# Kernel tuning notes

Hardware: AMD Instinct MI355X
Metric: run time of the kernel (lower is better)

Reference implementation:

```python
import jax, jax.numpy as jnp
import numpy as np

BS, L, D, N, K = 2048, 100, 256, 16, 32
M_CONST = 2
NEG = -1e9


def setup_inputs() -> dict:
    key = jax.random.key(0)
    ks = jax.random.split(key, 6)
    hist = jax.random.normal(ks[0], (BS, L, D), dtype=jnp.float32)
    hist_mask = jnp.ones((BS, L), dtype=jnp.float32)  # passed but unused by PolyAttention (faithful)
    cand = jax.random.normal(ks[1], (BS, N, D), dtype=jnp.float32)
    num_interests = jax.random.randint(ks[2], (BS,), 1, K + 1, dtype=jnp.int32)
    cat_counts = jax.random.randint(ks[3], (BS,), 1, 21, dtype=jnp.int32)
    W_poly = jax.random.normal(ks[4], (D, D), dtype=jnp.float32) * (1.0 / np.sqrt(D))
    context_codes = jax.random.normal(ks[5], (K, D), dtype=jnp.float32) * (1.0 / np.sqrt(D))
    return {
        "history_news_representations": hist,
        "history_mask": hist_mask,
        "candidate_news_representations": cand,
        "num_extracted_interests": num_interests,
        "unique_category_counts": cat_counts,
        "W_poly": W_poly,
        "context_codes": context_codes,
    }


def _forward(hist, hist_mask, cand, num_interests, cat_counts, W_poly, context_codes):
    # --- PolyAttention ---
    proj = jnp.tanh(jnp.einsum("bld,ed->ble", hist, W_poly))        # [bs, L, ccd]
    weights = jnp.einsum("ble,ke->bkl", proj, context_codes)         # [bs, K, L]
    cc_mask = jnp.arange(K)[None, :] < num_interests[:, None]        # [bs, K]
    weights = jnp.where(cc_mask[:, :, None], weights, NEG)
    weights = jax.nn.softmax(weights, axis=2)
    weights = jnp.nan_to_num(weights, nan=0.0, posinf=0.0, neginf=0.0)
    interests = jnp.einsum("bkl,bld->bkd", weights, hist)            # [bs, K, d]

    # --- InterestCandidateAttention over all N candidates at once ---
    aw = jnp.einsum("bkd,bnd->bnk", interests, cand)                 # [bs, N, K]
    dyn_K = jnp.ceil(jnp.log2(M_CONST * cat_counts.astype(jnp.float32))).astype(jnp.int32)
    dyn_K = jnp.clip(dyn_K, 1, K)                                    # [bs]
    # rank of each entry in descending order along K
    order = jnp.argsort(-aw, axis=-1)
    rank = jnp.argsort(order, axis=-1)                               # [bs, N, K]
    topk_mask = (rank < dyn_K[:, None, None]).astype(aw.dtype)
    masked = aw * topk_mask
    user = jnp.einsum("bnk,bkd->bnd", masked, interests)             # [bs, N, d]
    return user


def reference(history_news_representations, history_mask, candidate_news_representations,
              num_extracted_interests, unique_category_counts, W_poly, context_codes):
    return _forward(history_news_representations, history_mask, candidate_news_representations,
                    num_extracted_interests, unique_category_counts, W_poly, context_codes)
```

## Files before the change

### kernel.cpp

```cpp
#include <hip/hip_runtime.h>
#include <math.h>

#define NEGV (-1e9f)

typedef _Float16 half8 __attribute__((ext_vector_type(8)));
typedef float f32x4 __attribute__((ext_vector_type(4)));


__device__ inline float tanh_fast(float x) {
    float t = __expf(2.0f * x);
    float r = __builtin_amdgcn_rcpf(t + 1.0f);
    return fmaf(-2.0f, r, 1.0f);
}

__device__ inline void split8(const float4 a, const float4 b, half8& h, half8& m) {
    const float* pa = (const float*)&a;
    const float* pb = (const float*)&b;
    #pragma unroll
    for (int q = 0; q < 4; ++q) {
        float x = pa[q];
        _Float16 hi = (_Float16)x;
        h[q] = hi; m[q] = (_Float16)(x - (float)hi);
    }
    #pragma unroll
    for (int q = 0; q < 4; ++q) {
        float x = pb[q];
        _Float16 hi = (_Float16)x;
        h[4+q] = hi; m[4+q] = (_Float16)(x - (float)hi);
    }
}

__global__ __launch_bounds__(256)
void k_prep(const float* __restrict__ W, const float* __restrict__ cc,
            half8* __restrict__ Wf, half8* __restrict__ Cf)
{
    int slot = blockIdx.x * 256 + threadIdx.x;
    if (slot < 8192) {
        int kt = slot >> 10;
        int ct = (slot >> 6) & 15;
        int lane = slot & 63;
        int e = ct * 16 + (lane & 15);
        int g = lane >> 4;
        const float* src = &W[(size_t)e * 256 + kt * 32 + g * 8];
        float4 a = *(const float4*)src;
        float4 b = *(const float4*)(src + 4);
        half8 h, m;
        split8(a, b, h, m);
        Wf[((kt * 2 + 0) * 16 + ct) * 64 + lane] = h;
        Wf[((kt * 2 + 1) * 16 + ct) * 64 + lane] = m;
    } else if (slot < 9216) {
        int s = slot - 8192;
        int lane = s & 63;
        int ct = (s >> 6) & 1;
        int et = s >> 7;
        int k2 = ct * 16 + (lane & 15);
        int g = lane >> 4;
        const float* src = &cc[(size_t)k2 * 256 + et * 32 + g * 8];
        float4 a = *(const float4*)src;
        float4 b = *(const float4*)(src + 4);
        half8 h, m;
        split8(a, b, h, m);
        Cf[((et * 2 + 0) * 2 + ct) * 64 + lane] = h;
        Cf[((et * 2 + 1) * 2 + ct) * 64 + lane] = m;
    }
}

__global__ __launch_bounds__(256, 2)
void k_proj_logits(const float* __restrict__ hist, const half8* __restrict__ Wf,
                   const half8* __restrict__ Cf, float* __restrict__ logits)
{
    __shared__ float Pj[128][68];

    const int tid  = threadIdx.x;
    const int lane = tid & 63;
    const int w    = tid >> 6;
    const int wr   = w >> 1, wc = w & 1;
    const int g    = lane >> 4;
    const int r    = lane & 15;
    const size_t rowBase = (size_t)blockIdx.x * 128;

    f32x4 acc[4][8];
    #pragma unroll
    for (int i = 0; i < 4; ++i)
        #pragma unroll
        for (int j = 0; j < 8; ++j) acc[i][j] = (f32x4)(0.0f);

    const float* aPtr = &hist[(rowBase + (size_t)wr * 64 + r) * 256 + g * 8];

    float4 a0[4], a1[4];
    #pragma unroll
    for (int rt = 0; rt < 4; ++rt) {
        const float* s = aPtr + rt * (16 * 256);
        a0[rt] = *(const float4*)s;
        a1[rt] = *(const float4*)(s + 4);
    }

    #pragma unroll
    for (int kt = 0; kt < 8; ++kt) {
        half8 Ah[4], Am[4];
        #pragma unroll
        for (int rt = 0; rt < 4; ++rt)
            split8(a0[rt], a1[rt], Ah[rt], Am[rt]);
        if (kt < 7) {
            #pragma unroll
            for (int rt = 0; rt < 4; ++rt) {
                const float* s = aPtr + rt * (16 * 256) + (kt + 1) * 32;
                a0[rt] = *(const float4*)s;
                a1[rt] = *(const float4*)(s + 4);
            }
        }
        #pragma unroll
        for (int ct = 0; ct < 8; ++ct) {
            int ctg = wc * 8 + ct;
            half8 Bh = Wf[(size_t)((kt * 2 + 0) * 16 + ctg) * 64 + lane];
            half8 Bm = Wf[(size_t)((kt * 2 + 1) * 16 + ctg) * 64 + lane];
            #pragma unroll
            for (int rt = 0; rt < 4; ++rt) {
                acc[rt][ct] = __builtin_amdgcn_mfma_f32_16x16x32_f16(Ah[rt], Bh, acc[rt][ct], 0, 0, 0);
                acc[rt][ct] = __builtin_amdgcn_mfma_f32_16x16x32_f16(Ah[rt], Bm, acc[rt][ct], 0, 0, 0);
                acc[rt][ct] = __builtin_amdgcn_mfma_f32_16x16x32_f16(Am[rt], Bh, acc[rt][ct], 0, 0, 0);
            }
        }
    }

    f32x4 acc2[2][2];
    #pragma unroll
    for (int i = 0; i < 2; ++i)
        #pragma unroll
        for (int j = 0; j < 2; ++j) acc2[i][j] = (f32x4)(0.0f);

    #pragma unroll
    for (int ec = 0; ec < 4; ++ec) {
        __syncthreads();
        if (wc == (ec >> 1)) {
            #pragma unroll
            for (int rt = 0; rt < 4; ++rt) {
                #pragma unroll
                for (int c4i = 0; c4i < 4; ++c4i) {
                    int ctm = (ec & 1) * 4 + c4i;
                    f32x4 t = acc[rt][ctm];
                    int el = c4i * 16 + r;
                    int rb = 64 * wr + rt * 16 + g * 4;
                    #pragma unroll
                    for (int i = 0; i < 4; ++i)
                        Pj[rb + i][el] = tanh_fast(t[i]);
                }
            }
        }
        __syncthreads();
        #pragma unroll
        for (int ks = 0; ks < 2; ++ks) {
            half8 Ah2[2], Am2[2];
            #pragma unroll
            for (int rt2 = 0; rt2 < 2; ++rt2) {
                const float* src = &Pj[32 * w + rt2 * 16 + r][ks * 32 + g * 8];
                float4 p0 = *(const float4*)src;
                float4 p1 = *(const float4*)(src + 4);
                split8(p0, p1, Ah2[rt2], Am2[rt2]);
            }
            int et = ec * 2 + ks;
            #pragma unroll
            for (int ct = 0; ct < 2; ++ct) {
                half8 Bh = Cf[((et * 2 + 0) * 2 + ct) * 64 + lane];
                half8 Bm = Cf[((et * 2 + 1) * 2 + ct) * 64 + lane];
                #pragma unroll
                for (int rt2 = 0; rt2 < 2; ++rt2) {
                    acc2[rt2][ct] = __builtin_amdgcn_mfma_f32_16x16x32_f16(Ah2[rt2], Bh, acc2[rt2][ct], 0, 0, 0);
                    acc2[rt2][ct] = __builtin_amdgcn_mfma_f32_16x16x32_f16(Ah2[rt2], Bm, acc2[rt2][ct], 0, 0, 0);
                    acc2[rt2][ct] = __builtin_amdgcn_mfma_f32_16x16x32_f16(Am2[rt2], Bh, acc2[rt2][ct], 0, 0, 0);
                }
            }
        }
    }
    #pragma unroll
    for (int rt2 = 0; rt2 < 2; ++rt2)
        #pragma unroll
        for (int ct = 0; ct < 2; ++ct)
            #pragma unroll
            for (int i = 0; i < 4; ++i) {
                size_t grow = rowBase + 32 * w + rt2 * 16 + g * 4 + i;
                logits[grow * 32 + ct * 16 + r] = acc2[rt2][ct][i];
            }
}

__global__ __launch_bounds__(256, 3)
void k_attn(const float* __restrict__ hist, const float* __restrict__ cand,
            const int* __restrict__ numi, const int* __restrict__ catc,
            const float* __restrict__ logits, float* __restrict__ out)
{
    __shared__ float wT[100][36];
    __shared__ float ints[32][260];
    __shared__ float aws[16][36];
    __shared__ float maw[16][36];

    const int tid = threadIdx.x;
    const int b = blockIdx.x;
    const int num = numi[b];

    for (int idx = tid; idx < 3200; idx += 256) {
        int l = idx >> 5;
        int k = idx & 31;
        wT[l][k] = logits[(size_t)b * 3200 + idx];
    }
    __syncthreads();

    {
        const int k = tid >> 3;
        const int lg = tid & 7;
        const bool valid = k < num;
        float vals[13];
        float m = -INFINITY;
        #pragma unroll
        for (int i = 0; i < 13; ++i) {
            int l = lg + 8 * i;
            if (l < 100) {
                float v = valid ? wT[l][k] : NEGV;
                vals[i] = v;
                m = fmaxf(m, v);
            }
        }
        #pragma unroll
        for (int off = 1; off < 8; off <<= 1)
            m = fmaxf(m, __shfl_xor(m, off, 8));
        float s = 0.0f;
        #pragma unroll
        for (int i = 0; i < 13; ++i) {
            int l = lg + 8 * i;
            if (l < 100) {
                float e = expf(vals[i] - m);
                s += e;
                wT[l][k] = e;
            }
        }
        #pragma unroll
        for (int off = 1; off < 8; off <<= 1)
            s += __shfl_xor(s, off, 8);
        float inv = 1.0f / s;
        #pragma unroll
        for (int i = 0; i < 13; ++i) {
            int l = lg + 8 * i;
            if (l < 100) wT[l][k] *= inv;
        }
    }
    __syncthreads();

    {
        const int dq = tid & 63;
        const int kh = tid >> 6;
        float4 a4[8];
        #pragma unroll
        for (int kk = 0; kk < 8; ++kk) { a4[kk].x = a4[kk].y = a4[kk].z = a4[kk].w = 0.0f; }
        const float4* hrow = (const float4*)&hist[(size_t)b * 25600] + dq;
        #pragma unroll 4
        for (int l = 0; l < 100; ++l) {
            float4 hv = hrow[(size_t)l * 64];
            float4 w0 = *(const float4*)&wT[l][8 * kh];
            float4 w1 = *(const float4*)&wT[l][8 * kh + 4];
            float wv[8] = {w0.x, w0.y, w0.z, w0.w, w1.x, w1.y, w1.z, w1.w};
            #pragma unroll
            for (int kk = 0; kk < 8; ++kk) {
                a4[kk].x = fmaf(wv[kk], hv.x, a4[kk].x);
                a4[kk].y = fmaf(wv[kk], hv.y, a4[kk].y);
                a4[kk].z = fmaf(wv[kk], hv.z, a4[kk].z);
                a4[kk].w = fmaf(wv[kk], hv.w, a4[kk].w);
            }
        }
        #pragma unroll
        for (int kk = 0; kk < 8; ++kk)
            *(float4*)&ints[8 * kh + kk][4 * dq] = a4[kk];
    }
    __syncthreads();

    {
        const int n = tid & 15;
        const int kq = tid >> 4;
        const float4* cg = (const float4*)&cand[((size_t)b * 16 + n) * 256];
        const float4* i0 = (const float4*)&ints[kq][0];
        const float4* i1 = (const float4*)&ints[kq + 16][0];
        float s0 = 0.0f, s1 = 0.0f;
        for (int q = 0; q < 64; ++q) {
            float4 cv = cg[q];
            float4 v0 = i0[q];
            float4 v1 = i1[q];
            s0 += v0.x * cv.x + v0.y * cv.y + v0.z * cv.z + v0.w * cv.w;
            s1 += v1.x * cv.x + v1.y * cv.y + v1.z * cv.z + v1.w * cv.w;
        }
        aws[n][kq] = s0;
        aws[n][kq + 16] = s1;
    }
    __syncthreads();

    {
        int c = catc[b];
        int dynK = 32 - __clz(2 * c - 1);
        const int k = tid & 31;
        const int n1 = tid >> 5;
        #pragma unroll
        for (int h = 0; h < 2; ++h) {
            int n = n1 + 8 * h;
            float a = aws[n][k];
            int cnt = 0;
            #pragma unroll
            for (int j = 0; j < 32; ++j) {
                float aj = aws[n][j];
                cnt += (aj > a) || (aj == a && j < k);
            }
            maw[n][k] = (cnt < dynK) ? a : 0.0f;
        }
    }
    __syncthreads();

    {
        const int dd = tid & 63;
        const int ng = tid >> 6;
        float4 acc4[4];
        #pragma unroll
        for (int nn = 0; nn < 4; ++nn) { acc4[nn].x = acc4[nn].y = acc4[nn].z = acc4[nn].w = 0.0f; }
        for (int k = 0; k < 32; ++k) {
            float4 iv = *(const float4*)&ints[k][4 * dd];
            #pragma unroll
            for (int nn = 0; nn < 4; ++nn) {
                float m = maw[4 * ng + nn][k];
                acc4[nn].x = fmaf(m, iv.x, acc4[nn].x);
                acc4[nn].y = fmaf(m, iv.y, acc4[nn].y);
                acc4[nn].z = fmaf(m, iv.z, acc4[nn].z);
                acc4[nn].w = fmaf(m, iv.w, acc4[nn].w);
            }
        }
        #pragma unroll
        for (int nn = 0; nn < 4; ++nn) {
            *(float4*)&out[((size_t)b * 16 + 4 * ng + nn) * 256 + 4 * dd] = acc4[nn];
        }
    }
}

extern "C" void kernel_launch(void* const* d_in, const int* in_sizes, int n_in,
                              void* d_out, int out_size, void* d_ws, size_t ws_size,
                              hipStream_t stream) {
    const float* hist = (const float*)d_in[0];
    const float* cand = (const float*)d_in[2];
    const int*   numi = (const int*)d_in[3];
    const int*   catc = (const int*)d_in[4];
    const float* W    = (const float*)d_in[5];
    const float* cc   = (const float*)d_in[6];
    float* out = (float*)d_out;
    float* logits = (float*)d_ws;
    const size_t LOG_BYTES = 26214400;
    const size_t WF_BYTES = 262144;
    const size_t CF_BYTES = 32768;
    char* fragBase = (ws_size >= LOG_BYTES + WF_BYTES + CF_BYTES)
                     ? ((char*)d_ws + LOG_BYTES)
                     : (char*)d_out;
    half8* Wf = (half8*)fragBase;
    half8* Cf = (half8*)(fragBase + WF_BYTES);

    k_prep<<<36, 256, 0, stream>>>(W, cc, Wf, Cf);
    k_proj_logits<<<1600, 256, 0, stream>>>(hist, Wf, Cf, logits);
    k_attn<<<2048, 256, 0, stream>>>(hist, cand, numi, catc, logits, out);
}
```

Before: 265.7 us.

## Double-buffer W tiles in LDS via async global_load_lds in projection GEMM

The projection kernel now streams the pre-split fp16 W_poly tiles into a 64KB double-buffered LDS region with direct global-to-LDS loads, prefetching the next k-tile while MFMAs consume the current one. Previously each wave read the B fragments straight from global memory. The A-operand register prefetch is also double-buffered through a macro-expanded loop with explicit waitcnt and barriers. The enlarged shared buffer may reduce occupancy. Separately, the interest-aggregation loop unroll goes from 4 to 10.

Measured after the change: 243.3 us. -8.4%, faster.

```diff
diff --git a/kernel.cpp b/kernel.cpp
--- a/kernel.cpp
+++ b/kernel.cpp
@@ -28,6 +28,12 @@
         _Float16 hi = (_Float16)x;
         h[4+q] = hi; m[4+q] = (_Float16)(x - (float)hi);
     }
+}
+
+__device__ inline void gload_lds16(const void* g, void* lds) {
+    __builtin_amdgcn_global_load_lds(
+        (const __attribute__((address_space(1))) unsigned int*)g,
+        (__attribute__((address_space(3))) unsigned int*)lds, 16, 0, 0);
 }
 
 __global__ __launch_bounds__(256)
@@ -65,11 +71,53 @@
     }
 }
 
+#define K1_BODY(KT, CURBUF, RS0, RS1, RD0, RD1, LAST)                              \
+    {                                                                              \
+        if (!(LAST)) {                                                             \
+            const char* s_ = wsrc + (size_t)((KT) + 1) * 32768;                    \
+            char* d_ = smem + ((CURBUF) ^ 1) * 32768 + ldsW;                       \
+            _Pragma("unroll")                                                      \
+            for (int i = 0; i < 8; ++i)                                            \
+                gload_lds16(s_ + i * 4096, d_ + i * 4096);                         \
+        }                                                                          \
+        __builtin_amdgcn_sched_barrier(0);                                         \
+        if (!(LAST)) {                                                             \
+            _Pragma("unroll")                                                      \
+            for (int rt = 0; rt < 4; ++rt) {                                       \
+                const float* s_ = aPtr + rt * (16 * 256) + ((KT) + 1) * 32;        \
+                RD0[rt] = *(const float4*)s_;                                      \
+                RD1[rt] = *(const float4*)(s_ + 4);                                \
+            }                                                                      \
+        }                                                                          \
+        half8 Ah[4], Am[4];                                                        \
+        _Pragma("unroll")                                                          \
+        for (int rt = 0; rt < 4; ++rt)                                             \
+            split8(RS0[rt], RS1[rt], Ah[rt], Am[rt]);                              \
+        const _Float16* Bf = (const _Float16*)(smem + (CURBUF) * 32768);           \
+        _Pragma("unroll")                                                          \
+        for (int ct = 0; ct < 8; ++ct) {                                           \
+            int ctg = wc * 8 + ct;                                                 \
+            half8 Bh = *(const half8*)&Bf[(( 0 + ctg) * 64 + lane) * 8];           \
+            half8 Bm = *(const half8*)&Bf[((16 + ctg) * 64 + lane) * 8];           \
+            _Pragma("unroll")                                                      \
+            for (int rt = 0; rt < 4; ++rt) {                                       \
+                acc[rt][ct] = __builtin_amdgcn_mfma_f32_16x16x32_f16(Ah[rt], Bh, acc[rt][ct], 0, 0, 0); \
+                acc[rt][ct] = __builtin_amdgcn_mfma_f32_16x16x32_f16(Ah[rt], Bm, acc[rt][ct], 0, 0, 0); \
+                acc[rt][ct] = __builtin_amdgcn_mfma_f32_16x16x32_f16(Am[rt], Bh, acc[rt][ct], 0, 0, 0); \
+            }                                                                      \
+        }                                                                          \
+        __builtin_amdgcn_sched_barrier(0);                                         \
+        asm volatile("s_waitcnt vmcnt(8)" ::: "memory");                           \
+        __builtin_amdgcn_s_barrier();                                              \
+        __builtin_amdgcn_sched_barrier(0);                                         \
+    }
+
 __global__ __launch_bounds__(256, 2)
 void k_proj_logits(const float* __restrict__ hist, const half8* __restrict__ Wf,
                    const half8* __restrict__ Cf, float* __restrict__ logits)
 {
-    __shared__ float Pj[128][68];
+    __shared__ __align__(16) char smem[65536];
+    float (*Pj)[68] = (float(*)[68])smem;
 
     const int tid  = threadIdx.x;
     const int lane = tid & 63;
@@ -86,41 +134,27 @@
         for (int j = 0; j < 8; ++j) acc[i][j] = (f32x4)(0.0f);
 
     const float* aPtr = &hist[(rowBase + (size_t)wr * 64 + r) * 256 + g * 8];
-
-    float4 a0[4], a1[4];
+    const char*  wsrc = (const char*)Wf + tid * 16;
+    const int    ldsW = (tid & 192) * 16;
+
+    float4 rA0[4], rA1[4], rB0[4], rB1[4];
     #pragma unroll
     for (int rt = 0; rt < 4; ++rt) {
         const float* s = aPtr + rt * (16 * 256);
-        a0[rt] = *(const float4*)s;
-        a1[rt] = *(const float4*)(s + 4);
-    }
-
-    #pragma unroll
-    for (int kt = 0; kt < 8; ++kt) {
-        half8 Ah[4], Am[4];
-        #pragma unroll
-        for (int rt = 0; rt < 4; ++rt)
-            split8(a0[rt], a1[rt], Ah[rt], Am[rt]);
-        if (kt < 7) {
-            #pragma unroll
-            for (int rt = 0; rt < 4; ++rt) {
-                const float* s = aPtr + rt * (16 * 256) + (kt + 1) * 32;
-                a0[rt] = *(const float4*)s;
-                a1[rt] = *(const float4*)(s + 4);
-            }
-        }
-        #pragma unroll
-        for (int ct = 0; ct < 8; ++ct) {
-            int ctg = wc * 8 + ct;
-            half8 Bh = Wf[(size_t)((kt * 2 + 0) * 16 + ctg) * 64 + lane];
-            half8 Bm = Wf[(size_t)((kt * 2 + 1) * 16 + ctg) * 64 + lane];
-            #pragma unroll
-            for (int rt = 0; rt < 4; ++rt) {
-                acc[rt][ct] = __builtin_amdgcn_mfma_f32_16x16x32_f16(Ah[rt], Bh, acc[rt][ct], 0, 0, 0);
-                acc[rt][ct] = __builtin_amdgcn_mfma_f32_16x16x32_f16(Ah[rt], Bm, acc[rt][ct], 0, 0, 0);
-                acc[rt][ct] = __builtin_amdgcn_mfma_f32_16x16x32_f16(Am[rt], Bh, acc[rt][ct], 0, 0, 0);
-            }
-        }
+        rA0[rt] = *(const float4*)s;
+        rA1[rt] = *(const float4*)(s + 4);
+    }
+    #pragma unroll
+    for (int i = 0; i < 8; ++i)
+        gload_lds16(wsrc + i * 4096, smem + ldsW + i * 4096);
+    __builtin_amdgcn_sched_barrier(0);
+    asm volatile("s_waitcnt vmcnt(0)" ::: "memory");
+    __builtin_amdgcn_s_barrier();
+    __builtin_amdgcn_sched_barrier(0);
+
+    for (int kt2 = 0; kt2 < 4; ++kt2) {
+        K1_BODY(2 * kt2,     0, rA0, rA1, rB0, rB1, false);
+        K1_BODY(2 * kt2 + 1, 1, rB0, rB1, rA0, rA1, (kt2 == 3));
     }
 
     f32x4 acc2[2][2];
@@ -251,7 +285,7 @@
         #pragma unroll
         for (int kk = 0; kk < 8; ++kk) { a4[kk].x = a4[kk].y = a4[kk].z = a4[kk].w = 0.0f; }
         const float4* hrow = (const float4*)&hist[(size_t)b * 25600] + dq;
-        #pragma unroll 4
+        #pragma unroll 10
         for (int l = 0; l < 100; ++l) {
             float4 hv = hrow[(size_t)l * 64];
             float4 w0 = *(const float4*)&wT[l][8 * kh];
```

## Restructure projection kernel with register-resident W and async LDS-pipelined history tiles

Applied to the files above, without the earlier changes.

The projection+logits kernel now runs 512-thread blocks over 256 rows, processed in four 64-row chunks. Each wave keeps its 32-column slice of the split-fp16 W fragments in registers, and history tiles stream into a triple-buffered, XOR-swizzled LDS ring via global_load_lds with explicit vmcnt waits. The full 64x256 tanh projection is staged in LDS before the context-code GEMM, and the context-code fragments are also preloaded into LDS. The goal is to remove redundant W reloads from global memory and overlap history loads with MFMA work, at the cost of heavy register pressure (128 half8 values) and hand-managed barriers. The attention kernel's history loop unroll is also raised from 4 to 10.

New measurement: 308.7 us. 1.16x slower.

```diff
diff --git a/kernel.cpp b/kernel.cpp
--- a/kernel.cpp
+++ b/kernel.cpp
@@ -28,6 +28,12 @@
         _Float16 hi = (_Float16)x;
         h[4+q] = hi; m[4+q] = (_Float16)(x - (float)hi);
     }
+}
+
+__device__ inline void gload_lds16(const void* g, void* lds) {
+    __builtin_amdgcn_global_load_lds(
+        (const __attribute__((address_space(1))) unsigned int*)g,
+        (__attribute__((address_space(3))) unsigned int*)lds, 16, 0, 0);
 }
 
 __global__ __launch_bounds__(256)
@@ -65,122 +71,144 @@
     }
 }
 
-__global__ __launch_bounds__(256, 2)
+__global__ __launch_bounds__(512, 2)
 void k_proj_logits(const float* __restrict__ hist, const half8* __restrict__ Wf,
                    const half8* __restrict__ Cf, float* __restrict__ logits)
 {
-    __shared__ float Pj[128][68];
+    __shared__ __align__(16) char smem[24576 + 66560 + 32768];
+    char* As = smem;
+    float (*Pj)[260] = (float(*)[260])(smem + 24576);
+    _Float16* CfL = (_Float16*)(smem + 24576 + 66560);
 
     const int tid  = threadIdx.x;
     const int lane = tid & 63;
     const int w    = tid >> 6;
-    const int wr   = w >> 1, wc = w & 1;
     const int g    = lane >> 4;
     const int r    = lane & 15;
-    const size_t rowBase = (size_t)blockIdx.x * 128;
-
-    f32x4 acc[4][8];
+    const size_t rowBase = (size_t)blockIdx.x * 256;
+
+    half8 WB[2][2][8];
     #pragma unroll
-    for (int i = 0; i < 4; ++i)
-        #pragma unroll
-        for (int j = 0; j < 8; ++j) acc[i][j] = (f32x4)(0.0f);
-
-    const float* aPtr = &hist[(rowBase + (size_t)wr * 64 + r) * 256 + g * 8];
-
-    float4 a0[4], a1[4];
+    for (int kt = 0; kt < 8; ++kt)
+        #pragma unroll
+        for (int spl = 0; spl < 2; ++spl)
+            #pragma unroll
+            for (int ctl = 0; ctl < 2; ++ctl)
+                WB[ctl][spl][kt] = Wf[(size_t)((kt * 2 + spl) * 16 + (2 * w + ctl)) * 64 + lane];
+
+    {
+        const char* cs = (const char*)Cf;
+        char* cd = (char*)CfL;
+        const int wb = w * 1024;
+        #pragma unroll
+        for (int j = 0; j < 4; ++j)
+            gload_lds16(cs + j * 8192 + wb + lane * 16, cd + j * 8192 + wb);
+    }
+
+    const int arow = tid >> 3;
+    const int alow = (tid & 7) ^ (arow & 7);
+    const float* aSrc = hist + (rowBase + arow) * 256 + (alow >> 1) * 8 + (alow & 1) * 4;
+    char* aDstU = As + w * 1024;
+
+    gload_lds16((const void*)(aSrc + 0),  aDstU + 0 * 8192);
+    gload_lds16((const void*)(aSrc + 32), aDstU + 1 * 8192);
+    __builtin_amdgcn_sched_barrier(0);
+    asm volatile("s_waitcnt vmcnt(0)" ::: "memory");
+    __builtin_amdgcn_s_barrier();
+
+    f32x4 acc[4][2];
     #pragma unroll
-    for (int rt = 0; rt < 4; ++rt) {
-        const float* s = aPtr + rt * (16 * 256);
-        a0[rt] = *(const float4*)s;
-        a1[rt] = *(const float4*)(s + 4);
-    }
-
-    #pragma unroll
-    for (int kt = 0; kt < 8; ++kt) {
-        half8 Ah[4], Am[4];
+    for (int rt = 0; rt < 4; ++rt) { acc[rt][0] = (f32x4)(0.0f); acc[rt][1] = (f32x4)(0.0f); }
+
+    int sb = 0;
+    int aOff = 0;
+    for (int c = 0; c < 4; ++c) {
+        char* P0 = As + sb * 8192;
+        int sb1 = sb + 1; if (sb1 >= 3) sb1 -= 3;
+        int sb2 = sb + 2; if (sb2 >= 3) sb2 -= 3;
+        char* P1 = As + sb1 * 8192;
+        char* P2 = As + sb2 * 8192;
+        char* D0 = aDstU + sb * 8192;
+        char* D1 = aDstU + sb1 * 8192;
+        char* D2 = aDstU + sb2 * 8192;
+        const int nextAOff = (c < 3) ? aOff + 16384 : aOff;
+
+        #pragma unroll
+        for (int kt = 0; kt < 8; ++kt) {
+            {
+                int so = (kt <= 5) ? (aOff + (kt + 2) * 32) : (nextAOff + (kt - 6) * 32);
+                char* d = (kt % 3 == 0) ? D2 : ((kt % 3 == 1) ? D0 : D1);
+                gload_lds16((const void*)(aSrc + so), d);
+            }
+            __builtin_amdgcn_sched_barrier(0);
+            const char* Ab = (kt % 3 == 0) ? P0 : ((kt % 3 == 1) ? P1 : P2);
+            float4 v0[4], v1[4];
+            #pragma unroll
+            for (int rt = 0; rt < 4; ++rt) {
+                int row = rt * 16 + r;
+                int u0 = (row * 8) + ((g * 2) ^ (row & 7));
+                v0[rt] = *(const float4*)(Ab + u0 * 16);
+                v1[rt] = *(const float4*)(Ab + (u0 ^ 1) * 16);
+            }
+            #pragma unroll
+            for (int rt = 0; rt < 4; ++rt) {
+                half8 Ah, Am;
+                split8(v0[rt], v1[rt], Ah, Am);
+                acc[rt][0] = __builtin_amdgcn_mfma_f32_16x16x32_f16(Ah, WB[0][0][kt], acc[rt][0], 0, 0, 0);
+                acc[rt][0] = __builtin_amdgcn_mfma_f32_16x16x32_f16(Ah, WB[0][1][kt], acc[rt][0], 0, 0, 0);
+                acc[rt][0] = __builtin_amdgcn_mfma_f32_16x16x32_f16(Am, WB[0][0][kt], acc[rt][0], 0, 0, 0);
+                acc[rt][1] = __builtin_amdgcn_mfma_f32_16x16x32_f16(Ah, WB[1][0][kt], acc[rt][1], 0, 0, 0);
+                acc[rt][1] = __builtin_amdgcn_mfma_f32_16x16x32_f16(Ah, WB[1][1][kt], acc[rt][1], 0, 0, 0);
+                acc[rt][1] = __builtin_amdgcn_mfma_f32_16x16x32_f16(Am, WB[1][0][kt], acc[rt][1], 0, 0, 0);
+            }
+            __builtin_amdgcn_sched_barrier(0);
+            asm volatile("s_waitcnt vmcnt(1)" ::: "memory");
+            __builtin_amdgcn_s_barrier();
+        }
+
         #pragma unroll
         for (int rt = 0; rt < 4; ++rt)
-            split8(a0[rt], a1[rt], Ah[rt], Am[rt]);
-        if (kt < 7) {
-            #pragma unroll
-            for (int rt = 0; rt < 4; ++rt) {
-                const float* s = aPtr + rt * (16 * 256) + (kt + 1) * 32;
-                a0[rt] = *(const float4*)s;
-                a1[rt] = *(const float4*)(s + 4);
-            }
-        }
-        #pragma unroll
-        for (int ct = 0; ct < 8; ++ct) {
-            int ctg = wc * 8 + ct;
-            half8 Bh = Wf[(size_t)((kt * 2 + 0) * 16 + ctg) * 64 + lane];
-            half8 Bm = Wf[(size_t)((kt * 2 + 1) * 16 + ctg) * 64 + lane];
-            #pragma unroll
-            for (int rt = 0; rt < 4; ++rt) {
-                acc[rt][ct] = __builtin_amdgcn_mfma_f32_16x16x32_f16(Ah[rt], Bh, acc[rt][ct], 0, 0, 0);
-                acc[rt][ct] = __builtin_amdgcn_mfma_f32_16x16x32_f16(Ah[rt], Bm, acc[rt][ct], 0, 0, 0);
-                acc[rt][ct] = __builtin_amdgcn_mfma_f32_16x16x32_f16(Am[rt], Bh, acc[rt][ct], 0, 0, 0);
-            }
-        }
-    }
-
-    f32x4 acc2[2][2];
-    #pragma unroll
-    for (int i = 0; i < 2; ++i)
-        #pragma unroll
-        for (int j = 0; j < 2; ++j) acc2[i][j] = (f32x4)(0.0f);
-
-    #pragma unroll
-    for (int ec = 0; ec < 4; ++ec) {
-        __syncthreads();
-        if (wc == (ec >> 1)) {
-            #pragma unroll
-            for (int rt = 0; rt < 4; ++rt) {
+            #pragma unroll
+            for (int ctl = 0; ctl < 2; ++ctl) {
+                f32x4 t4 = acc[rt][ctl];
+                int e = w * 32 + ctl * 16 + r;
+                int rowb = rt * 16 + g * 4;
                 #pragma unroll
-                for (int c4i = 0; c4i < 4; ++c4i) {
-                    int ctm = (ec & 1) * 4 + c4i;
-                    f32x4 t = acc[rt][ctm];
-                    int el = c4i * 16 + r;
-                    int rb = 64 * wr + rt * 16 + g * 4;
-                    #pragma unroll
-                    for (int i = 0; i < 4; ++i)
-                        Pj[rb + i][el] = tanh_fast(t[i]);
-                }
-            }
-        }
-        __syncthreads();
-        #pragma unroll
-        for (int ks = 0; ks < 2; ++ks) {
-            half8 Ah2[2], Am2[2];
-            #pragma unroll
-            for (int rt2 = 0; rt2 < 2; ++rt2) {
-                const float* src = &Pj[32 * w + rt2 * 16 + r][ks * 32 + g * 8];
-                float4 p0 = *(const float4*)src;
-                float4 p1 = *(const float4*)(src + 4);
-                split8(p0, p1, Ah2[rt2], Am2[rt2]);
-            }
-            int et = ec * 2 + ks;
-            #pragma unroll
-            for (int ct = 0; ct < 2; ++ct) {
-                half8 Bh = Cf[((et * 2 + 0) * 2 + ct) * 64 + lane];
-                half8 Bm = Cf[((et * 2 + 1) * 2 + ct) * 64 + lane];
-                #pragma unroll
-                for (int rt2 = 0; rt2 < 2; ++rt2) {
-                    acc2[rt2][ct] = __builtin_amdgcn_mfma_f32_16x16x32_f16(Ah2[rt2], Bh, acc2[rt2][ct], 0, 0, 0);
-                    acc2[rt2][ct] = __builtin_amdgcn_mfma_f32_16x16x32_f16(Ah2[rt2], Bm, acc2[rt2][ct], 0, 0, 0);
-                    acc2[rt2][ct] = __builtin_amdgcn_mfma_f32_16x16x32_f16(Am2[rt2], Bh, acc2[rt2][ct], 0, 0, 0);
-                }
-            }
-        }
-    }
-    #pragma unroll
-    for (int rt2 = 0; rt2 < 2; ++rt2)
-        #pragma unroll
-        for (int ct = 0; ct < 2; ++ct)
+                for (int i = 0; i < 4; ++i)
+                    Pj[rowb + i][e] = tanh_fast(t4[i]);
+                acc[rt][ctl] = (f32x4)(0.0f);
+            }
+        asm volatile("s_waitcnt lgkmcnt(0)" ::: "memory");
+        __builtin_amdgcn_s_barrier();
+        {
+            const int rt2 = w >> 1;
+            const int cte = w & 1;
+            f32x4 acc2 = (f32x4)(0.0f);
+            #pragma unroll
+            for (int kt2 = 0; kt2 < 8; ++kt2) {
+                const float* ps = &Pj[rt2 * 16 + r][kt2 * 32 + g * 8];
+                float4 p0 = *(const float4*)ps;
+                float4 p1 = *(const float4*)(ps + 4);
+                half8 Ah2, Am2;
+                split8(p0, p1, Ah2, Am2);
+                half8 Bh = *(const half8*)&CfL[(size_t)(((kt2 * 2 + 0) * 2 + cte) * 64 + lane) * 8];
+                half8 Bm = *(const half8*)&CfL[(size_t)(((kt2 * 2 + 1) * 2 + cte) * 64 + lane) * 8];
+                acc2 = __builtin_amdgcn_mfma_f32_16x16x32_f16(Ah2, Bh, acc2, 0, 0, 0);
+                acc2 = __builtin_amdgcn_mfma_f32_16x16x32_f16(Ah2, Bm, acc2, 0, 0, 0);
+                acc2 = __builtin_amdgcn_mfma_f32_16x16x32_f16(Am2, Bh, acc2, 0, 0, 0);
+            }
             #pragma unroll
             for (int i = 0; i < 4; ++i) {
-                size_t grow = rowBase + 32 * w + rt2 * 16 + g * 4 + i;
-                logits[grow * 32 + ct * 16 + r] = acc2[rt2][ct][i];
-            }
+                size_t grow = rowBase + c * 64 + rt2 * 16 + g * 4 + i;
+                logits[grow * 32 + cte * 16 + r] = acc2[i];
+            }
+        }
+        asm volatile("s_waitcnt lgkmcnt(0)" ::: "memory");
+        __builtin_amdgcn_s_barrier();
+
+        sb += 2; if (sb >= 3) sb -= 3;
+        aOff += 16384;
+    }
 }
 
 __global__ __launch_bounds__(256, 3)
@@ -251,7 +279,7 @@
         #pragma unroll
         for (int kk = 0; kk < 8; ++kk) { a4[kk].x = a4[kk].y = a4[kk].z = a4[kk].w = 0.0f; }
         const float4* hrow = (const float4*)&hist[(size_t)b * 25600] + dq;
-        #pragma unroll 4
+        #pragma unroll 10
         for (int l = 0; l < 100; ++l) {
             float4 hv = hrow[(size_t)l * 64];
             float4 w0 = *(const float4*)&wT[l][8 * kh];
@@ -355,6 +383,6 @@
     half8* Cf = (half8*)(fragBase + WF_BYTES);
 
     k_prep<<<36, 256, 0, stream>>>(W, cc, Wf, Cf);
-    k_proj_logits<<<1600, 256, 0, stream>>>(hist, Wf, Cf, logits);
+    k_proj_logits<<<800, 512, 0, stream>>>(hist, Wf, Cf, logits);
     k_attn<<<2048, 256, 0, stream>>>(hist, cand, numi, catc, logits, out);
 }
```
